# Optimization experiments

Hardware: AMD Instinct MI355X
Metric: run time of the kernel (lower is better)

Reference implementation:

```python
import jax, jax.numpy as jnp
import numpy as np

B, S, HID = 4, 8192, 1024
H, D = 16, 64
CHUNK = 64
N_BEFORE, N_AFTER = 1, 0
MASK_VALUE = -1e9


def look_adjacent(x, n_before, n_after):
    # x: [B, H, n_chunks, chunk, ...] -> concat rolled neighbor chunks along chunk-len dim
    if n_before == 0 and n_after == 0:
        return x
    slices = [jnp.roll(x, shift=-i, axis=2) for i in range(-n_before, n_after + 1)]
    return jnp.concatenate(slices, axis=3)


def setup_inputs() -> dict:
    key = jax.random.key(0)
    k0, k1, k2, k3 = jax.random.split(key, 4)
    scale = 1.0 / np.sqrt(HID)
    return {
        "hidden_states": jax.random.normal(k0, (B, S, HID), dtype=jnp.float32),
        "Wq": jax.random.normal(k1, (HID, HID), dtype=jnp.float32) * scale,
        "Wk": jax.random.normal(k2, (HID, HID), dtype=jnp.float32) * scale,
        "Wv": jax.random.normal(k3, (HID, HID), dtype=jnp.float32) * scale,
    }


def reference(hidden_states, Wq, Wk, Wv):
    b, s, _ = hidden_states.shape
    nC = s // CHUNK

    def split_heads(x):  # [B,S,HID] -> [B,H,S,D]
        return x.reshape(b, s, H, D).transpose(0, 2, 1, 3)

    q = split_heads(hidden_states @ Wq)
    k = split_heads(hidden_states @ Wk) / jnp.sqrt(jnp.asarray(D, hidden_states.dtype))
    v = split_heads(hidden_states @ Wv)

    # chunk: [B,H,nC,C,D]
    q = q.reshape(b, H, nC, CHUNK, D)
    k = k.reshape(b, H, nC, CHUNK, D)
    v = v.reshape(b, H, nC, CHUNK, D)

    idx = jnp.broadcast_to(jnp.arange(s), (b, H, s)).reshape(b, H, nC, CHUNK)
    q_idx = idx
    k_idx = look_adjacent(idx, N_BEFORE, N_AFTER)  # [B,H,nC,(1+nb+na)*C]
    k = look_adjacent(k, N_BEFORE, N_AFTER)        # [B,H,nC,(1+nb+na)*C,D]
    v = look_adjacent(v, N_BEFORE, N_AFTER)

    dots = jnp.einsum("bhncd,bhnkd->bhnck", q, k)  # [B,H,nC,C,K]
    causal = q_idx[..., :, None] >= k_idx[..., None, :]  # is_decoder causal mask
    dots = jnp.where(causal, dots, jnp.asarray(MASK_VALUE, dots.dtype))

    probs = jax.nn.softmax(dots, axis=-1)
    out = jnp.einsum("bhnck,bhnkd->bhncd", probs, v)  # [B,H,nC,C,D]
    out = out.reshape(b, H, s, D).transpose(0, 2, 1, 3).reshape(b, s, H * D)
    return out
```

## Files before the change

### kernel.cpp

```cpp
#include <hip/hip_runtime.h>
#include <hip/hip_bf16.h>

#define NB 4
#define NS 8192
#define NHID 1024
#define NH 16
#define ND 64
#define NCHUNK 128

typedef __attribute__((ext_vector_type(8))) __bf16 bf16x8;
typedef __attribute__((ext_vector_type(4))) float f32x4;

__device__ __forceinline__ unsigned short f2bf(float x) {
  unsigned int u = __builtin_bit_cast(unsigned int, x);
  unsigned int r = (u + 0x7FFFu + ((u >> 16) & 1u)) >> 16;
  return (unsigned short)r;
}

__device__ __forceinline__ void gload16(const void* g, void* l) {
  __builtin_amdgcn_global_load_lds(
      (const __attribute__((address_space(1))) unsigned int*)g,
      (__attribute__((address_space(3))) unsigned int*)l, 16, 0, 0);
}

__global__ __launch_bounds__(256) void convert_x(const float* __restrict__ x,
                                                 unsigned short* __restrict__ xb) {
  int gt = blockIdx.x * 256 + threadIdx.x;
  const float4* xf = (const float4*)x;
  float4 v0 = xf[gt * 2 + 0];
  float4 v1 = xf[gt * 2 + 1];
  uint4 o;
  o.x = f2bf(v0.x) | ((unsigned)f2bf(v0.y) << 16);
  o.y = f2bf(v0.z) | ((unsigned)f2bf(v0.w) << 16);
  o.z = f2bf(v1.x) | ((unsigned)f2bf(v1.y) << 16);
  o.w = f2bf(v1.z) | ((unsigned)f2bf(v1.w) << 16);
  ((uint4*)xb)[gt] = o;
}

__global__ __launch_bounds__(256) void transpose_w(const float* __restrict__ w0,
                                                   const float* __restrict__ w1,
                                                   const float* __restrict__ w2,
                                                   unsigned short* __restrict__ wt) {
  __shared__ float tile[32][33];
  int wi = blockIdx.z;
  const float* w = (wi == 0) ? w0 : ((wi == 1) ? w1 : w2);
  float scale = (wi == 1) ? 0.125f : 1.0f;
  int k0 = blockIdx.x * 32, n0 = blockIdx.y * 32;
  int tx = threadIdx.x, ty = threadIdx.y;
#pragma unroll
  for (int i = 0; i < 4; i++)
    tile[ty + i * 8][tx] = w[(k0 + ty + i * 8) * NHID + n0 + tx];
  __syncthreads();
#pragma unroll
  for (int i = 0; i < 4; i++)
    wt[(wi * NHID + n0 + ty + i * 8) * NHID + k0 + tx] =
        f2bf(tile[tx][ty + i * 8] * scale);
}

__global__ __launch_bounds__(256, 2) void gemm_qkv(
    const unsigned short* __restrict__ xb, const unsigned short* __restrict__ wt,
    unsigned short* __restrict__ qg, unsigned short* __restrict__ kg,
    unsigned short* __restrict__ vg) {
  __shared__ alignas(16) unsigned short As[128 * 32];
  __shared__ alignas(16) unsigned short Bs[128 * 32];
  int bn = blockIdx.x, bm = blockIdx.y;
  int t = threadIdx.x;
  int w = t >> 6, l = t & 63, lg = l >> 4, lm = l & 15;
  int wr = w >> 1, wc = w & 1;
  f32x4 acc[4][4] = {};

  for (int kt = 0; kt < NHID / 32; ++kt) {
    int k0 = kt * 32;
    __syncthreads();
#pragma unroll
    for (int i = 0; i < 2; i++) {
      int g = t + i * 256;
      int row = g >> 2, cc = g & 3;
      gload16(xb + (size_t)(bm * 128 + row) * NHID + k0 + cc * 8,
              (char*)As + g * 16);
      gload16(wt + (size_t)(bn * 128 + row) * NHID + k0 + cc * 8,
              (char*)Bs + g * 16);
    }
    __syncthreads();
    bf16x8 av[4], bv[4];
#pragma unroll
    for (int mi = 0; mi < 4; mi++) {
      int row = wr * 64 + mi * 16 + lm;
      av[mi] = *reinterpret_cast<const bf16x8*>(&As[row * 32 + lg * 8]);
    }
#pragma unroll
    for (int ni = 0; ni < 4; ni++) {
      int row = wc * 64 + ni * 16 + lm;
      bv[ni] = *reinterpret_cast<const bf16x8*>(&Bs[row * 32 + lg * 8]);
    }
#pragma unroll
    for (int mi = 0; mi < 4; mi++)
#pragma unroll
      for (int ni = 0; ni < 4; ni++)
        acc[mi][ni] = __builtin_amdgcn_mfma_f32_16x16x32_bf16(
            av[mi], bv[ni], acc[mi][ni], 0, 0, 0);
  }

  int gn0 = bn * 128;
  int wsel = gn0 >> 10;
  unsigned short* dst = (wsel == 0) ? qg : ((wsel == 1) ? kg : vg);
#pragma unroll
  for (int mi = 0; mi < 4; mi++)
#pragma unroll
    for (int ni = 0; ni < 4; ni++)
#pragma unroll
      for (int r = 0; r < 4; r++) {
        int gm = bm * 128 + wr * 64 + mi * 16 + lg * 4 + r;
        int gn = gn0 + wc * 64 + ni * 16 + lm;
        int b = gm >> 13, s = gm & (NS - 1);
        int h = (gn >> 6) & (NH - 1), d = gn & (ND - 1);
        dst[(((size_t)(b * NH + h) * NS) + s) * ND + d] = f2bf(acc[mi][ni][r]);
      }
}

__global__ __launch_bounds__(256, 2) void attn_local(
    const unsigned short* __restrict__ qg, const unsigned short* __restrict__ kg,
    const unsigned short* __restrict__ vg, float* __restrict__ out) {
  __shared__ alignas(16) unsigned short qs[64 * 64];
  __shared__ alignas(16) unsigned short ks2[128 * 64];
  __shared__ alignas(16) unsigned short vts[64 * 128];
  __shared__ alignas(16) unsigned short ps[64 * 128];
  int c = blockIdx.x, h = blockIdx.y, b = blockIdx.z;
  int t = threadIdx.x;
  int w = t >> 6, l = t & 63, lg = l >> 4, lm = l & 15;
  size_t bhbase = (size_t)(b * NH + h) * NS * ND;
  int kv0 = (c - 1) * 64;

#pragma unroll
  for (int i = 0; i < 2; i++) {
    int g = t + i * 256;
    int row = g >> 3, cc = g & 7;
    uint4 v = *reinterpret_cast<const uint4*>(qg + bhbase +
                                              (size_t)(c * 64 + row) * ND + cc * 8);
    int byte = (row * 128 + cc * 16) ^ ((row & 7) << 4);
    *reinterpret_cast<uint4*>((char*)qs + byte) = v;
  }
#pragma unroll
  for (int i = 0; i < 4; i++) {
    int g = t + i * 256;
    int row = g >> 3, cc = g & 7;
    int s = kv0 + row;
    if (s < 0) s = 0;
    uint4 v = *reinterpret_cast<const uint4*>(kg + bhbase + (size_t)s * ND + cc * 8);
    int byte = (row * 128 + cc * 16) ^ ((row & 7) << 4);
    *reinterpret_cast<uint4*>((char*)ks2 + byte) = v;
  }
  {
    int k = t >> 1, half = t & 1;
    int s = kv0 + k;
    if (s < 0) s = 0;
#pragma unroll
    for (int i = 0; i < 4; i++) {
      int d0 = half * 32 + i * 8;
      uint4 v = *reinterpret_cast<const uint4*>(vg + bhbase + (size_t)s * ND + d0);
      unsigned int u[4] = {v.x, v.y, v.z, v.w};
#pragma unroll
      for (int j = 0; j < 8; j++) {
        unsigned short val = (unsigned short)(u[j >> 1] >> ((j & 1) * 16));
        vts[(d0 + j) * 128 + (k ^ (j << 3))] = val;
      }
    }
  }
  __syncthreads();

  bf16x8 qa[2];
#pragma unroll
  for (int ks = 0; ks < 2; ks++) {
    int row = w * 16 + lm;
    int byte = (row * 128 + (ks * 32 + lg * 8) * 2) ^ ((row & 7) << 4);
    qa[ks] = *reinterpret_cast<const bf16x8*>((char*)qs + byte);
  }
  f32x4 sf[8];
#pragma unroll
  for (int nt = 0; nt < 8; nt++) {
    f32x4 a = {};
#pragma unroll
    for (int ks = 0; ks < 2; ks++) {
      int n = nt * 16 + lm;
      int byte = (n * 128 + (ks * 32 + lg * 8) * 2) ^ ((n & 7) << 4);
      bf16x8 kb = *reinterpret_cast<const bf16x8*>((char*)ks2 + byte);
      a = __builtin_amdgcn_mfma_f32_16x16x32_bf16(qa[ks], kb, a, 0, 0, 0);
    }
    sf[nt] = a;
  }

  float mx[4] = {-1e30f, -1e30f, -1e30f, -1e30f};
#pragma unroll
  for (int nt = 0; nt < 8; nt++) {
    int j = nt * 16 + lm;
#pragma unroll
    for (int r = 0; r < 4; r++) {
      int q = w * 16 + lg * 4 + r;
      bool valid = (j <= q + 64) && (c > 0 || j >= 64);
      if (valid) mx[r] = fmaxf(mx[r], sf[nt][r]);
    }
  }
#pragma unroll
  for (int r = 0; r < 4; r++)
#pragma unroll
    for (int d = 1; d < 16; d <<= 1) mx[r] = fmaxf(mx[r], __shfl_xor(mx[r], d, 64));

  float sum[4] = {0.f, 0.f, 0.f, 0.f};
#pragma unroll
  for (int nt = 0; nt < 8; nt++) {
    int j = nt * 16 + lm;
#pragma unroll
    for (int r = 0; r < 4; r++) {
      int q = w * 16 + lg * 4 + r;
      bool valid = (j <= q + 64) && (c > 0 || j >= 64);
      float p = valid ? __expf(sf[nt][r] - mx[r]) : 0.0f;
      sf[nt][r] = p;
      sum[r] += p;
    }
  }
#pragma unroll
  for (int r = 0; r < 4; r++)
#pragma unroll
    for (int d = 1; d < 16; d <<= 1) sum[r] += __shfl_xor(sum[r], d, 64);

#pragma unroll
  for (int nt = 0; nt < 8; nt++) {
    int j = nt * 16 + lm;
#pragma unroll
    for (int r = 0; r < 4; r++) {
      int q = w * 16 + lg * 4 + r;
      int byte = (q * 256 + j * 2) ^ ((q & 7) << 4);
      *reinterpret_cast<unsigned short*>((char*)ps + byte) = f2bf(sf[nt][r]);
    }
  }
  __syncthreads();

  bf16x8 pa[4];
#pragma unroll
  for (int ks = 0; ks < 4; ks++) {
    int q = w * 16 + lm;
    int byte = (q * 256 + (ks * 32 + lg * 8) * 2) ^ ((q & 7) << 4);
    pa[ks] = *reinterpret_cast<const bf16x8*>((char*)ps + byte);
  }
  float rcpl[4];
#pragma unroll
  for (int r = 0; r < 4; r++) rcpl[r] = 1.0f / sum[r];
#pragma unroll
  for (int nt = 0; nt < 4; nt++) {
    f32x4 o = {};
#pragma unroll
    for (int ks = 0; ks < 4; ks++) {
      int dn = nt * 16 + lm;
      int byte = (dn * 256 + (ks * 32 + lg * 8) * 2) ^ ((dn & 7) << 4);
      bf16x8 vb = *reinterpret_cast<const bf16x8*>((char*)vts + byte);
      o = __builtin_amdgcn_mfma_f32_16x16x32_bf16(pa[ks], vb, o, 0, 0, 0);
    }
#pragma unroll
    for (int r = 0; r < 4; r++) {
      int sq = c * 64 + w * 16 + lg * 4 + r;
      int d = nt * 16 + lm;
      out[(size_t)(b * NS + sq) * (NH * ND) + h * ND + d] = o[r] * rcpl[r];
    }
  }
}

extern "C" void kernel_launch(void* const* d_in, const int* in_sizes, int n_in,
                              void* d_out, int out_size, void* d_ws, size_t ws_size,
                              hipStream_t stream) {
  const float* hs = (const float*)d_in[0];
  const float* wq = (const float*)d_in[1];
  const float* wk = (const float*)d_in[2];
  const float* wv = (const float*)d_in[3];
  float* out = (float*)d_out;
  char* ws = (char*)d_ws;

  const size_t XB_BYTES = (size_t)NB * NS * NHID * 2;
  const size_t WT_BYTES = (size_t)3 * NHID * NHID * 2;
  const size_t QKV_BYTES = (size_t)NB * NH * NS * ND * 2;
  unsigned short* xb = (unsigned short*)ws;
  unsigned short* wt = (unsigned short*)(ws + XB_BYTES);
  unsigned short* qg = (unsigned short*)(ws + XB_BYTES + WT_BYTES);
  unsigned short* kg = (unsigned short*)(ws + XB_BYTES + WT_BYTES + QKV_BYTES);
  unsigned short* vg = (unsigned short*)(ws + XB_BYTES + WT_BYTES + 2 * QKV_BYTES);

  hipLaunchKernelGGL(convert_x, dim3((NB * NS * NHID) / (256 * 8)), dim3(256), 0,
                     stream, hs, xb);
  hipLaunchKernelGGL(transpose_w, dim3(32, 32, 3), dim3(32, 8), 0, stream, wq, wk,
                     wv, wt);
  hipLaunchKernelGGL(gemm_qkv, dim3(3 * NHID / 128, (NB * NS) / 128), dim3(256), 0,
                     stream, xb, wt, qg, kg, vg);
  hipLaunchKernelGGL(attn_local, dim3(NCHUNK, NH, NB), dim3(256), 0, stream, qg, kg,
                     vg, out);
}
```

Measured before the change: 538.2 us.

## Rework QKV GEMM with 256x256 tiles, double-buffered LDS and XCD-aware block remap

The QKV projection GEMM now uses 512-thread blocks computing 256x256 tiles with a K-step of 64. LDS is double-buffered, with a swizzled layout and explicit vmcnt waits so the next tile loads while MFMAs run; setprio and a remap of block IDs across the eight XCDs are added. The attention kernel aliases the P buffer onto the Q/K LDS region to cut shared memory and allow 4 blocks per CU, and it prefetches V into registers early, deferring the transpose store. The cost is higher register pressure and an extra barrier in attention, and the 128KB LDS footprint limits GEMM occupancy.

```diff
diff --git a/kernel.cpp b/kernel.cpp
--- a/kernel.cpp
+++ b/kernel.cpp
@@ -57,79 +57,129 @@
         f2bf(tile[tx][ty + i * 8] * scale);
 }
 
-__global__ __launch_bounds__(256, 2) void gemm_qkv(
+__device__ __forceinline__ void stage_tile(const unsigned short* __restrict__ src,
+                                           size_t row0, int kt, char* ldst,
+                                           int tid) {
+#pragma unroll
+  for (int i = 0; i < 4; i++) {
+    int g = tid + i * 512;
+    int r = g >> 3;
+    int slot = (g & 7) ^ (r & 7);
+    gload16(src + (row0 + r) * NHID + kt * 64 + slot * 8, ldst + g * 16);
+  }
+}
+
+__global__ __launch_bounds__(512, 2) void gemm_qkv(
     const unsigned short* __restrict__ xb, const unsigned short* __restrict__ wt,
     unsigned short* __restrict__ qg, unsigned short* __restrict__ kg,
     unsigned short* __restrict__ vg) {
-  __shared__ alignas(16) unsigned short As[128 * 32];
-  __shared__ alignas(16) unsigned short Bs[128 * 32];
-  int bn = blockIdx.x, bm = blockIdx.y;
-  int t = threadIdx.x;
-  int w = t >> 6, l = t & 63, lg = l >> 4, lm = l & 15;
-  int wr = w >> 1, wc = w & 1;
-  f32x4 acc[4][4] = {};
-
-  for (int kt = 0; kt < NHID / 32; ++kt) {
-    int k0 = kt * 32;
-    __syncthreads();
-#pragma unroll
-    for (int i = 0; i < 2; i++) {
-      int g = t + i * 256;
-      int row = g >> 2, cc = g & 3;
-      gload16(xb + (size_t)(bm * 128 + row) * NHID + k0 + cc * 8,
-              (char*)As + g * 16);
-      gload16(wt + (size_t)(bn * 128 + row) * NHID + k0 + cc * 8,
-              (char*)Bs + g * 16);
-    }
-    __syncthreads();
-    bf16x8 av[4], bv[4];
-#pragma unroll
-    for (int mi = 0; mi < 4; mi++) {
-      int row = wr * 64 + mi * 16 + lm;
-      av[mi] = *reinterpret_cast<const bf16x8*>(&As[row * 32 + lg * 8]);
-    }
-#pragma unroll
-    for (int ni = 0; ni < 4; ni++) {
-      int row = wc * 64 + ni * 16 + lm;
-      bv[ni] = *reinterpret_cast<const bf16x8*>(&Bs[row * 32 + lg * 8]);
-    }
-#pragma unroll
-    for (int mi = 0; mi < 4; mi++)
-#pragma unroll
-      for (int ni = 0; ni < 4; ni++)
-        acc[mi][ni] = __builtin_amdgcn_mfma_f32_16x16x32_bf16(
-            av[mi], bv[ni], acc[mi][ni], 0, 0, 0);
-  }
-
-  int gn0 = bn * 128;
-  int wsel = gn0 >> 10;
+  __shared__ alignas(16) char smem[131072];
+  int bid = blockIdx.x;
+  int wg = (bid & 7) * 192 + (bid >> 3);
+  int bm = wg / 12, bn = wg % 12;
+  int tid = threadIdx.x;
+  int l = tid & 63, lg = l >> 4, lm = l & 15;
+  int w = tid >> 6, wm = w >> 2, wn = w & 3;
+
+  const size_t arow0 = (size_t)bm * 256;
+  const size_t brow0 = (size_t)bn * 256;
+
+  stage_tile(xb, arow0, 0, smem + 0, tid);
+  stage_tile(wt, brow0, 0, smem + 65536, tid);
+  stage_tile(xb, arow0, 1, smem + 32768, tid);
+  stage_tile(wt, brow0, 1, smem + 98304, tid);
+  asm volatile("s_waitcnt vmcnt(8)" ::: "memory");
+  __builtin_amdgcn_s_barrier();
+  asm volatile("" ::: "memory");
+
+  f32x4 acc[8][4] = {};
+
+  for (int t = 0; t < 16; ++t) {
+    const char* Ab = smem + (t & 1) * 32768;
+    const char* Bb = smem + 65536 + (t & 1) * 32768;
+    bf16x8 av[8][2], bv[4][2];
+#pragma unroll
+    for (int mi = 0; mi < 8; mi++)
+#pragma unroll
+      for (int ks = 0; ks < 2; ks++) {
+        int row = wm * 128 + mi * 16 + lm;
+        int byte = (row * 128 + ks * 64 + lg * 16) ^ ((row & 7) << 4);
+        av[mi][ks] = *reinterpret_cast<const bf16x8*>(Ab + byte);
+      }
+#pragma unroll
+    for (int ni = 0; ni < 4; ni++)
+#pragma unroll
+      for (int ks = 0; ks < 2; ks++) {
+        int row = wn * 64 + ni * 16 + lm;
+        int byte = (row * 128 + ks * 64 + lg * 16) ^ ((row & 7) << 4);
+        bv[ni][ks] = *reinterpret_cast<const bf16x8*>(Bb + byte);
+      }
+#pragma unroll
+    for (int q = 0; q < 4; q++) {
+      __builtin_amdgcn_s_setprio(1);
+#pragma unroll
+      for (int mi = 2 * q; mi < 2 * q + 2; mi++)
+#pragma unroll
+        for (int ni = 0; ni < 4; ni++)
+#pragma unroll
+          for (int ks = 0; ks < 2; ks++)
+            acc[mi][ni] = __builtin_amdgcn_mfma_f32_16x16x32_bf16(
+                av[mi][ks], bv[ni][ks], acc[mi][ni], 0, 0, 0);
+      __builtin_amdgcn_s_setprio(0);
+    }
+    asm volatile("s_waitcnt lgkmcnt(0)" ::: "memory");
+    __builtin_amdgcn_s_barrier();
+    asm volatile("" ::: "memory");
+    if (t < 14) {
+      stage_tile(xb, arow0, t + 2, (char*)smem + (t & 1) * 32768, tid);
+      stage_tile(wt, brow0, t + 2, (char*)smem + 65536 + (t & 1) * 32768, tid);
+      asm volatile("s_waitcnt vmcnt(8)" ::: "memory");
+    } else {
+      asm volatile("s_waitcnt vmcnt(0)" ::: "memory");
+    }
+    __builtin_amdgcn_s_barrier();
+    asm volatile("" ::: "memory");
+  }
+
+  int wsel = bn >> 2;
   unsigned short* dst = (wsel == 0) ? qg : ((wsel == 1) ? kg : vg);
-#pragma unroll
-  for (int mi = 0; mi < 4; mi++)
+  int n0 = (bn & 3) * 256;
+#pragma unroll
+  for (int mi = 0; mi < 8; mi++)
 #pragma unroll
     for (int ni = 0; ni < 4; ni++)
 #pragma unroll
       for (int r = 0; r < 4; r++) {
-        int gm = bm * 128 + wr * 64 + mi * 16 + lg * 4 + r;
-        int gn = gn0 + wc * 64 + ni * 16 + lm;
+        int gm = bm * 256 + wm * 128 + mi * 16 + lg * 4 + r;
+        int n = n0 + wn * 64 + ni * 16 + lm;
         int b = gm >> 13, s = gm & (NS - 1);
-        int h = (gn >> 6) & (NH - 1), d = gn & (ND - 1);
+        int h = n >> 6, d = n & (ND - 1);
         dst[(((size_t)(b * NH + h) * NS) + s) * ND + d] = f2bf(acc[mi][ni][r]);
       }
 }
 
-__global__ __launch_bounds__(256, 2) void attn_local(
+__global__ __launch_bounds__(256, 4) void attn_local(
     const unsigned short* __restrict__ qg, const unsigned short* __restrict__ kg,
     const unsigned short* __restrict__ vg, float* __restrict__ out) {
-  __shared__ alignas(16) unsigned short qs[64 * 64];
-  __shared__ alignas(16) unsigned short ks2[128 * 64];
-  __shared__ alignas(16) unsigned short vts[64 * 128];
-  __shared__ alignas(16) unsigned short ps[64 * 128];
+  __shared__ alignas(16) char lds[40960];
+  unsigned short* qs = (unsigned short*)lds;
+  unsigned short* ks2 = (unsigned short*)(lds + 8192);
+  unsigned short* vts = (unsigned short*)(lds + 24576);
+  char* psb = lds;
   int c = blockIdx.x, h = blockIdx.y, b = blockIdx.z;
   int t = threadIdx.x;
   int w = t >> 6, l = t & 63, lg = l >> 4, lm = l & 15;
   size_t bhbase = (size_t)(b * NH + h) * NS * ND;
   int kv0 = (c - 1) * 64;
+
+  int kq = t >> 1, half = t & 1;
+  int sv = kv0 + kq;
+  if (sv < 0) sv = 0;
+  uint4 vreg[4];
+#pragma unroll
+  for (int i = 0; i < 4; i++)
+    vreg[i] = *reinterpret_cast<const uint4*>(vg + bhbase + (size_t)sv * ND +
+                                              half * 32 + i * 8);
 
 #pragma unroll
   for (int i = 0; i < 2; i++) {
@@ -138,7 +188,7 @@
     uint4 v = *reinterpret_cast<const uint4*>(qg + bhbase +
                                               (size_t)(c * 64 + row) * ND + cc * 8);
     int byte = (row * 128 + cc * 16) ^ ((row & 7) << 4);
-    *reinterpret_cast<uint4*>((char*)qs + byte) = v;
+    *reinterpret_cast<uint4*>(lds + byte) = v;
   }
 #pragma unroll
   for (int i = 0; i < 4; i++) {
@@ -148,23 +198,7 @@
     if (s < 0) s = 0;
     uint4 v = *reinterpret_cast<const uint4*>(kg + bhbase + (size_t)s * ND + cc * 8);
     int byte = (row * 128 + cc * 16) ^ ((row & 7) << 4);
-    *reinterpret_cast<uint4*>((char*)ks2 + byte) = v;
-  }
-  {
-    int k = t >> 1, half = t & 1;
-    int s = kv0 + k;
-    if (s < 0) s = 0;
-#pragma unroll
-    for (int i = 0; i < 4; i++) {
-      int d0 = half * 32 + i * 8;
-      uint4 v = *reinterpret_cast<const uint4*>(vg + bhbase + (size_t)s * ND + d0);
-      unsigned int u[4] = {v.x, v.y, v.z, v.w};
-#pragma unroll
-      for (int j = 0; j < 8; j++) {
-        unsigned short val = (unsigned short)(u[j >> 1] >> ((j & 1) * 16));
-        vts[(d0 + j) * 128 + (k ^ (j << 3))] = val;
-      }
-    }
+    *reinterpret_cast<uint4*>(lds + 8192 + byte) = v;
   }
   __syncthreads();
 
@@ -223,6 +257,8 @@
 #pragma unroll
     for (int d = 1; d < 16; d <<= 1) sum[r] += __shfl_xor(sum[r], d, 64);
 
+  __syncthreads();
+
 #pragma unroll
   for (int nt = 0; nt < 8; nt++) {
     int j = nt * 16 + lm;
@@ -230,7 +266,20 @@
     for (int r = 0; r < 4; r++) {
       int q = w * 16 + lg * 4 + r;
       int byte = (q * 256 + j * 2) ^ ((q & 7) << 4);
-      *reinterpret_cast<unsigned short*>((char*)ps + byte) = f2bf(sf[nt][r]);
+      *reinterpret_cast<unsigned short*>(psb + byte) = f2bf(sf[nt][r]);
+    }
+  }
+  {
+    unsigned short* vtse = (unsigned short*)vts;
+#pragma unroll
+    for (int i = 0; i < 4; i++) {
+      int d0 = half * 32 + i * 8;
+      unsigned int u[4] = {vreg[i].x, vreg[i].y, vreg[i].z, vreg[i].w};
+#pragma unroll
+      for (int j = 0; j < 8; j++) {
+        unsigned short val = (unsigned short)(u[j >> 1] >> ((j & 1) * 16));
+        vtse[(d0 + j) * 128 + (kq ^ (j << 3))] = val;
+      }
     }
   }
   __syncthreads();
@@ -240,7 +289,7 @@
   for (int ks = 0; ks < 4; ks++) {
     int q = w * 16 + lm;
     int byte = (q * 256 + (ks * 32 + lg * 8) * 2) ^ ((q & 7) << 4);
-    pa[ks] = *reinterpret_cast<const bf16x8*>((char*)ps + byte);
+    pa[ks] = *reinterpret_cast<const bf16x8*>(psb + byte);
   }
   float rcpl[4];
 #pragma unroll
@@ -287,8 +336,8 @@
                      stream, hs, xb);
   hipLaunchKernelGGL(transpose_w, dim3(32, 32, 3), dim3(32, 8), 0, stream, wq, wk,
                      wv, wt);
-  hipLaunchKernelGGL(gemm_qkv, dim3(3 * NHID / 128, (NB * NS) / 128), dim3(256), 0,
-                     stream, xb, wt, qg, kg, vg);
-  hipLaunchKernelGGL(attn_local, dim3(NCHUNK, NH, NB), dim3(256), 0, stream, qg, kg,
-                     vg, out);
-}
+  hipLaunchKernelGGL(gemm_qkv, dim3(128 * 12), dim3(512), 0, stream, xb, wt, qg,
+                     kg, vg);
+  hipLaunchKernelGGL(attn_local, dim3(NCHUNK, NH, NB), dim3(256), 0, stream, qg,
+                     kg, vg, out);
+}
```

After: 673.5 us. 25.1% more time.
